# Kernel optimization log

Measured on AMD Instinct MI355X. Metric: run time of the kernel, lower is better.

The kernel has to match this reference:

```python
import jax, jax.numpy as jnp
import numpy as np

NPG = 39      # nodes per graph, from (1+8+64+9)*(39+1)=3280 = lin1 in_features
NEG_SLOPE = 0.2


def gat_conv(x, src, dst, W, a_src, a_dst, b, n):
    """PyG GATConv, heads=1, self-loops already appended to (src, dst).
    x:[N,Fin] W:[Fin,Fout] a_src/a_dst:[Fout] b:[Fout] -> [N,Fout]"""
    h = x @ W                                        # [N,Fout]
    e = jax.nn.leaky_relu(h[src] @ a_src + h[dst] @ a_dst, NEG_SLOPE)  # [E]
    m = jax.lax.stop_gradient(jax.ops.segment_max(e, dst, num_segments=n))
    w = jnp.exp(e - m[dst])
    denom = jax.ops.segment_sum(w, dst, num_segments=n)
    alpha = w / (denom[dst] + 1e-16)                 # segment softmax per target node
    out = jax.ops.segment_sum(alpha[:, None] * h[src], dst, num_segments=n)
    return out + b


def setup_inputs() -> dict:
    key = jax.random.key(0)
    ks = jax.random.split(key, 20)
    B, DEG = 4096, 8
    N = B * NPG
    E = N * DEG
    x = jax.random.normal(ks[0], (N, 1), dtype=jnp.float32)
    # block-diagonal edges: each node emits DEG edges to random nodes in SAME graph
    src = jnp.repeat(jnp.arange(N, dtype=jnp.int64), DEG)
    offs = (src // NPG) * NPG
    dst = offs + jax.random.randint(ks[1], (E,), 0, NPG, dtype=jnp.int64)
    edge_index = jnp.stack([src, dst])
    batch_vec = jnp.repeat(jnp.arange(B, dtype=jnp.int64), NPG)

    def glorot(k, shape):
        fan = shape[0] + (shape[1] if len(shape) > 1 else 1)
        s = jnp.sqrt(6.0 / fan)
        return jax.random.uniform(k, shape, jnp.float32, -s, s)

    p = {
        'W1': glorot(ks[2], (1, 8)),   'a1s': glorot(ks[3], (8,)),  'a1d': glorot(ks[4], (8,)),  'b1': jnp.zeros((8,), jnp.float32),
        'W2': glorot(ks[5], (8, 64)),  'a2s': glorot(ks[6], (64,)), 'a2d': glorot(ks[7], (64,)), 'b2': jnp.zeros((64,), jnp.float32),
        'W3': glorot(ks[8], (64, 9)),  'a3s': glorot(ks[9], (9,)),  'a3d': glorot(ks[10], (9,)), 'b3': jnp.zeros((9,), jnp.float32),
        'lW1': glorot(ks[11], (3280, 5000)), 'lb1': jnp.zeros((5000,), jnp.float32),
        'lW2': glorot(ks[12], (5000, 1024)), 'lb2': jnp.zeros((1024,), jnp.float32),
        'lW3': glorot(ks[13], (1024, 9)),    'lb3': jnp.zeros((9,), jnp.float32),
    }
    return {'x': x, 'edge_index': edge_index, 'batch_vec': batch_vec, **p}


def reference(x, edge_index, batch_vec,
              W1, a1s, a1d, b1, W2, a2s, a2d, b2, W3, a3s, a3d, b3,
              lW1, lb1, lW2, lb2, lW3, lb3):
    N = x.shape[0]
    B = N // NPG
    loops = jnp.arange(N, dtype=edge_index.dtype)
    src = jnp.concatenate([edge_index[0], loops])   # GATConv add_self_loops=True
    dst = jnp.concatenate([edge_index[1], loops])

    res = x.reshape(B, -1)                                    # [B,39]
    out0 = jax.ops.segment_max(x, batch_vec, num_segments=B)  # [B,1]

    h1 = jax.nn.relu(gat_conv(x, src, dst, W1, a1s, a1d, b1, N))   # dropout = eval no-op
    res1 = h1.reshape(B, -1)                                   # [B,312]
    out1 = jax.ops.segment_max(h1, batch_vec, num_segments=B)

    h2 = jax.nn.relu(gat_conv(h1, src, dst, W2, a2s, a2d, b2, N))
    res2 = h2.reshape(B, -1)                                   # [B,2496]
    out2 = jax.ops.segment_max(h2, batch_vec, num_segments=B)

    h3 = jax.nn.relu(gat_conv(h2, src, dst, W3, a3s, a3d, b3, N))
    res3 = h3.reshape(B, -1)                                   # [B,351]
    out3 = jax.ops.segment_max(h3, batch_vec, num_segments=B)

    f = jnp.concatenate([res, res1, res2, res3, out0, out1, out2, out3], axis=1)  # [B,3280]
    f = jax.nn.relu(f @ lW1 + lb1)
    f = jax.nn.relu(f @ lW2 + lb2)
    return f @ lW3 + lb3                                       # [B,9]
```

## Files before the change

### kernel.cpp

```cpp
#include <hip/hip_runtime.h>
#include <hip/hip_bf16.h>
#include <hip/hip_fp16.h>
#include <stdint.h>


typedef float f32x4 __attribute__((ext_vector_type(4)));
typedef short bf16x8 __attribute__((ext_vector_type(8)));

__device__ __forceinline__ unsigned fenc(float f) {
  int s = __float_as_int(f);
  return s < 0 ? ~(unsigned)s : ((unsigned)s | 0x80000000u);
}
__device__ __forceinline__ float fdec(unsigned u) {
  return (u & 0x80000000u) ? __int_as_float((int)(u & 0x7fffffffu))
                           : __int_as_float(~(int)u);
}


__global__ __launch_bounds__(128) void gnn_block(
    const float* __restrict__ x,
    const int* __restrict__ esrc, const int* __restrict__ edst,
    const float* __restrict__ W1, const float* __restrict__ a1s, const float* __restrict__ a1d, const float* __restrict__ b1,
    const float* __restrict__ W2, const float* __restrict__ a2s, const float* __restrict__ a2d, const float* __restrict__ b2,
    const float* __restrict__ W3, const float* __restrict__ a3s, const float* __restrict__ a3d, const float* __restrict__ b3,
    __hip_bfloat16* __restrict__ fA)
{
  __shared__ __align__(16) char HtU[5152];
  __shared__ __align__(16) __half h2buf[2574];
  __shared__ __align__(16) __half h1h[312];
  __shared__ float A[1599];
  __shared__ float den[40];
  __shared__ unsigned umax[40];
  __shared__ float sarr[40], darr[40], xbuf[40];
  __shared__ float a2buf[128];
  __shared__ unsigned umx[132];
  __shared__ float sW3s[576];

  const int tid = threadIdx.x, g = blockIdx.x;
  float* Hf  = (float*)HtU;
  __half* Hh = (__half*)HtU;

  const int rt = g >> 7, mi = (g >> 4) & 7, lrow = g & 15;
  const size_t gbase = (size_t)rt * 52 * 8192 + (size_t)(mi * 2) * 512 + (size_t)lrow * 8;
#define COLADDR(c) (gbase + (size_t)((c) >> 6) * 8192 + (size_t)(((c) >> 5) & 1) * 512 \
                    + (size_t)(((c) >> 3) & 3) * 128 + ((c) & 7))

  for (int i = tid; i < 576; i += 128) sW3s[i] = W3[i];
  a2buf[tid] = (tid < 64) ? a2s[tid] : a2d[tid - 64];
  for (int i = tid; i < 132; i += 128) umx[i] = 0u;
  for (int i = tid; i < 1599; i += 128) A[i] = 0.f;
  if (tid < 39) { den[tid] = 0.f; umax[tid] = 0u; }

  float xv = 0.f;
  if (tid < 39) { xv = x[g * 39 + tid]; xbuf[tid] = xv; fA[COLADDR(tid)] = __float2bfloat16(xv); }

  int els[3], eld[3];
  const int eb = g * 312, nb0 = g * 39;
#pragma unroll
  for (int it = 0; it < 3; ++it) {
    int e = it * 128 + tid, ls = -1, ld = 0;
    if (e < 351) {
      if (e < 312) { ls = esrc[eb + e] - nb0; ld = edst[eb + e] - nb0; }
      else         { ls = e - 312; ld = ls; }
    }
    els[it] = ls; eld[it] = ld;
  }
  float c_s = 0.f, c_d = 0.f;
  float w1r = W1[tid & 7], b1r = b1[tid & 7];
#pragma unroll
  for (int f = 0; f < 8; ++f) { float wv = W1[f]; c_s += wv * a1s[f]; c_d += wv * a1d[f]; }
  __syncthreads();

  if (tid < 39) atomicMax(&umx[0], fenc(xv));
  float ee[3];
#pragma unroll
  for (int it = 0; it < 3; ++it) {
    if (els[it] >= 0) {
      float e = xbuf[els[it]] * c_s + xbuf[eld[it]] * c_d;
      e = (e > 0.f) ? e : 0.2f * e;
      ee[it] = e;
      atomicMax(&umax[eld[it]], fenc(e));
    }
  }
  __syncthreads();
#pragma unroll
  for (int it = 0; it < 3; ++it) {
    if (els[it] >= 0) {
      float wv = __expf(ee[it] - fdec(umax[eld[it]]));
      atomicAdd(&den[eld[it]], wv);
      atomicAdd(&A[eld[it] * 41 + els[it]], wv);
    }
  }
  __syncthreads();
  if (tid < 39) {
    float q = 0.f;
#pragma unroll
    for (int k = 0; k < 39; ++k) q += A[tid * 41 + k] * xbuf[k];
    sarr[tid] = q * (1.f / (den[tid] + 1e-16f));
  }
  __syncthreads();
#pragma unroll
  for (int it = 0; it < 3; ++it) {
    int slot = it * 128 + tid;
    if (slot < 312) {
      int i = slot >> 3, fi = slot & 7;
      float v = fmaxf(sarr[i] * w1r + b1r, 0.f);
      h1h[slot] = __float2half(v);
      fA[COLADDR(39 + slot)] = __float2bfloat16(v);
      atomicMax(&umx[1 + fi], fenc(v));
    }
  }
  __syncthreads();

  {
    const int f = tid & 63, wv2 = tid >> 6;
    float w2k[8];
#pragma unroll
    for (int k = 0; k < 8; ++k) w2k[k] = W2[k * 64 + f];
    for (int it = 0; it < 20; ++it) {
      int i = it * 2 + wv2;
      if (i < 39) {
        float hv = 0.f;
#pragma unroll
        for (int k = 0; k < 8; ++k) hv += __half2float(h1h[i * 8 + k]) * w2k[k];
        Hh[i * 66 + f] = __float2half(hv);
      }
    }
    for (int i = tid; i < 1599; i += 128) A[i] = 0.f;
    if (tid < 39) { den[tid] = 0.f; umax[tid] = 0u; }
    __syncthreads();
    {
      int node = tid & 63;
      if (node < 39) {
        const float* ab = a2buf + (tid & 64);
        float s = 0.f;
#pragma unroll
        for (int f2 = 0; f2 < 64; ++f2) s += __half2float(Hh[node * 66 + f2]) * ab[f2];
        if (tid < 64) sarr[node] = s; else darr[node] = s;
      }
    }
    __syncthreads();
#pragma unroll
    for (int it = 0; it < 3; ++it) {
      if (els[it] >= 0) {
        float e = sarr[els[it]] + darr[eld[it]];
        e = (e > 0.f) ? e : 0.2f * e;
        ee[it] = e;
        atomicMax(&umax[eld[it]], fenc(e));
      }
    }
    __syncthreads();
#pragma unroll
    for (int it = 0; it < 3; ++it) {
      if (els[it] >= 0) {
        float wv = __expf(ee[it] - fdec(umax[eld[it]]));
        atomicAdd(&den[eld[it]], wv);
        atomicAdd(&A[eld[it] * 41 + els[it]], wv);
      }
    }
    __syncthreads();
    const float b2r = b2[f];
    for (int it = 0; it < 20; ++it) {
      int i = it * 2 + wv2;
      if (i < 39) {
        float inv = 1.f / (den[i] + 1e-16f);
        float acc = 0.f;
#pragma unroll
        for (int k = 0; k < 39; ++k) acc += A[i * 41 + k] * __half2float(Hh[k * 66 + f]);
        float v = fmaxf(acc * inv + b2r, 0.f);
        h2buf[i * 66 + f] = __float2half(v);
        fA[COLADDR(351 + i * 64 + f)] = __float2bfloat16(v);
        atomicMax(&umx[9 + f], fenc(v));
      }
    }
  }
  __syncthreads();

  {
#pragma unroll
    for (int it = 0; it < 3; ++it) {
      int slot = it * 128 + tid;
      if (slot < 351) {
        int i = slot / 9, f3 = slot - 9 * i;
        float acc = 0.f;
#pragma unroll
        for (int k = 0; k < 64; ++k) acc += __half2float(h2buf[i * 66 + k]) * sW3s[k * 9 + f3];
        Hf[i * 10 + f3] = acc;
      }
    }
    for (int i = tid; i < 1599; i += 128) A[i] = 0.f;
    if (tid < 39) { den[tid] = 0.f; umax[tid] = 0u; }
    __syncthreads();
    {
      int node = tid & 63;
      if (node < 39) {
        const float* av = (tid < 64) ? a3s : a3d;
        float s = 0.f;
#pragma unroll
        for (int f3 = 0; f3 < 9; ++f3) s += Hf[node * 10 + f3] * av[f3];
        if (tid < 64) sarr[node] = s; else darr[node] = s;
      }
    }
    __syncthreads();
#pragma unroll
    for (int it = 0; it < 3; ++it) {
      if (els[it] >= 0) {
        float e = sarr[els[it]] + darr[eld[it]];
        e = (e > 0.f) ? e : 0.2f * e;
        ee[it] = e;
        atomicMax(&umax[eld[it]], fenc(e));
      }
    }
    __syncthreads();
#pragma unroll
    for (int it = 0; it < 3; ++it) {
      if (els[it] >= 0) {
        float wv = __expf(ee[it] - fdec(umax[eld[it]]));
        atomicAdd(&den[eld[it]], wv);
        atomicAdd(&A[eld[it] * 41 + els[it]], wv);
      }
    }
    __syncthreads();
#pragma unroll
    for (int it = 0; it < 3; ++it) {
      int slot = it * 128 + tid;
      if (slot < 351) {
        int i = slot / 9, f3 = slot - 9 * i;
        float inv = 1.f / (den[i] + 1e-16f);
        float acc = 0.f;
#pragma unroll
        for (int k = 0; k < 39; ++k) acc += A[i * 41 + k] * Hf[k * 10 + f3];
        float v = fmaxf(acc * inv + b3[f3], 0.f);
        fA[COLADDR(2847 + slot)] = __float2bfloat16(v);
        atomicMax(&umx[73 + f3], fenc(v));
      }
    }
  }
  __syncthreads();

  if (tid < 130) {
    int c = 3198 + tid;
    float v = (tid < 82) ? fdec(umx[tid]) : 0.f;
    fA[COLADDR(c)] = __float2bfloat16(v);
  }
#undef COLADDR
}


__global__ __launch_bounds__(256) void conv_tiled(
    const float* __restrict__ W, short* __restrict__ WT,
    int K0, int N0, int KT)
{
  __shared__ float t[64][68];
  const int kb = blockIdx.x * 64, nb = blockIdx.y * 64;
  const int tid = threadIdx.x;
  const int tx = tid & 15, ty = tid >> 4;
#pragma unroll
  for (int r = 0; r < 4; ++r) {
    int k = kb + ty + r * 16, n = nb + tx * 4;
    float4 v = make_float4(0.f, 0.f, 0.f, 0.f);
    if (k < K0 && n < N0) v = *(const float4*)&W[(size_t)k * N0 + n];
    t[ty + r * 16][tx * 4 + 0] = v.x; t[ty + r * 16][tx * 4 + 1] = v.y;
    t[ty + r * 16][tx * 4 + 2] = v.z; t[ty + r * 16][tx * 4 + 3] = v.w;
  }
  __syncthreads();
  const int nl = tid >> 2, kc0 = tid & 3;
#pragma unroll
  for (int h = 0; h < 2; ++h) {
    int kc = kc0 + h * 4;
    int n = nb + nl, k = kb + kc * 8;
    union { bf16x8 v; __hip_bfloat16 b[8]; } z;
#pragma unroll
    for (int j = 0; j < 8; ++j) z.b[j] = __float2bfloat16(t[kc * 8 + j][nl]);
    int rt = n >> 7, mi = (n >> 4) & 7, lr = n & 15;
    int kt = k >> 6, kq = (k >> 5) & 1, lc = (k >> 3) & 3;
    size_t addr = ((((size_t)rt * KT) + kt) * 16 + mi * 2 + kq) * 512 + ((size_t)lr + 16 * lc) * 8;
    *(bf16x8*)&WT[addr] = z.v;
  }
}


__device__ __forceinline__ void gld_lds16(const void* gptr, void* l) {
  typedef const __attribute__((address_space(1))) unsigned int GU;
  typedef __attribute__((address_space(3))) unsigned int LU;
  __builtin_amdgcn_global_load_lds((GU*)gptr, (LU*)l, 16, 0, 0);
}

template<int MODE>
__global__ __launch_bounds__(256) void gemm_tiled(
    const short* __restrict__ A, const short* __restrict__ B,
    const float* __restrict__ bias, int Nreal,
    void* __restrict__ Cout, int Nn, int KT, int ktPerSplit, int outKT)
{
  __shared__ __align__(16) short lA[8192];
  __shared__ __align__(16) short lB[8192];
  const int tid = threadIdx.x;
  const int w = tid >> 6, L = tid & 63;
  const int lrow = L & 15, lch = L >> 4;
  const int mt = blockIdx.y, nt = blockIdx.x;
  const int mw = (w >> 1) * 4, nw = (w & 1) * 4;
  const int kt0 = blockIdx.z * ktPerSplit, kt1 = kt0 + ktPerSplit;

  const short* Ab = A + ((size_t)mt * KT) * 8192 + (size_t)L * 8;
  const short* Bb = B + ((size_t)nt * KT) * 8192 + (size_t)L * 8;

  f32x4 acc[4][4] = {};

  for (int kt = kt0; kt < kt1; ++kt) {
    const short* Ak = Ab + (size_t)kt * 8192;
    const short* Bk = Bb + (size_t)kt * 8192;
#pragma unroll
    for (int j = 0; j < 4; ++j) {
      int st = w * 4 + j;
      gld_lds16(Ak + st * 512, &lA[st * 512]);
      gld_lds16(Bk + st * 512, &lB[st * 512]);
    }
    __syncthreads();
#pragma unroll
    for (int kk = 0; kk < 2; ++kk) {
      bf16x8 af[4], bfr[4];
#pragma unroll
      for (int i = 0; i < 4; ++i) {
        af[i]  = *(const bf16x8*)&lA[((mw + i) * 2 + kk) * 512 + L * 8];
        bfr[i] = *(const bf16x8*)&lB[((nw + i) * 2 + kk) * 512 + L * 8];
      }
#pragma unroll
      for (int i = 0; i < 4; ++i)
#pragma unroll
        for (int j = 0; j < 4; ++j)
          acc[i][j] = __builtin_amdgcn_mfma_f32_16x16x32_bf16(af[i], bfr[j], acc[i][j], 0, 0, 0);
    }
    __syncthreads();
  }

  if (MODE == 0) {
    __hip_bfloat16* C = (__hip_bfloat16*)Cout;
#pragma unroll
    for (int j = 0; j < 4; ++j) {
      int n = nt * 128 + (nw + j) * 16 + lrow;
      float bn = (n < Nreal) ? bias[n] : 0.f;
      int kt = n >> 6, kq = (n >> 5) & 1, lc2 = (n >> 3) & 3, j2 = n & 7;
#pragma unroll
      for (int i = 0; i < 4; ++i) {
        int mi = mw + i;
        size_t base = ((((size_t)mt * outKT + kt) * 16) + mi * 2 + kq) * 512
                      + (size_t)(lch * 4) * 8 + (size_t)lc2 * 128 + j2;
#pragma unroll
        for (int r = 0; r < 4; ++r)
          C[base + r * 8] = __float2bfloat16(fmaxf(acc[i][j][r] + bn, 0.f));
      }
    }
  } else {
    float* P = (float*)Cout + (size_t)blockIdx.z * 4096 * 1024;
#pragma unroll
    for (int j = 0; j < 4; ++j) {
      int n = nt * 128 + (nw + j) * 16 + lrow;
#pragma unroll
      for (int i = 0; i < 4; ++i)
#pragma unroll
        for (int r = 0; r < 4; ++r) {
          int m = mt * 128 + (mw + i) * 16 + lch * 4 + r;
          P[(size_t)m * Nn + n] = acc[i][j][r];
        }
    }
  }
}


__global__ __launch_bounds__(256) void gemm3_fused(
    const float* __restrict__ P,
    const float* __restrict__ b2v,
    const float* __restrict__ W3,
    const float* __restrict__ b3v,
    float* __restrict__ out)
{
  __shared__ float sW3[9 * 1024];
  int tid = threadIdx.x;
  for (int i = tid; i < 9216; i += 256) { int k = i / 9, j = i - 9 * k; sW3[j * 1024 + k] = W3[i]; }
  __syncthreads();
  int row = blockIdx.x * 4 + (tid >> 6);
  int lane = tid & 63;
  const float* p0 = P + (size_t)row * 1024;
  const float* p1 = p0 + (size_t)4096 * 1024;
  float acc[9] = {0, 0, 0, 0, 0, 0, 0, 0, 0};
  for (int t = 0; t < 16; ++t) {
    int k = lane + 64 * t;
    float c = fmaxf(p0[k] + p1[k] + b2v[k], 0.f);
#pragma unroll
    for (int j = 0; j < 9; ++j) acc[j] += c * sW3[j * 1024 + k];
  }
#pragma unroll
  for (int j = 0; j < 9; ++j) {
    float v = acc[j];
    v += __shfl_down(v, 32, 64);
    v += __shfl_down(v, 16, 64);
    v += __shfl_down(v, 8, 64);
    v += __shfl_down(v, 4, 64);
    v += __shfl_down(v, 2, 64);
    v += __shfl_down(v, 1, 64);
    if (lane == 0) out[(size_t)row * 9 + j] = v + b3v[j];
  }
}


extern "C" void kernel_launch(void* const* d_in, const int* in_sizes, int n_in,
                              void* d_out, int out_size, void* d_ws, size_t ws_size,
                              hipStream_t stream)
{
  const float* x   = (const float*)d_in[0];
  const int*   ei  = (const int*)d_in[1];
  const float* W1  = (const float*)d_in[3];
  const float* a1s = (const float*)d_in[4];
  const float* a1d = (const float*)d_in[5];
  const float* b1  = (const float*)d_in[6];
  const float* W2  = (const float*)d_in[7];
  const float* a2s = (const float*)d_in[8];
  const float* a2d = (const float*)d_in[9];
  const float* b2  = (const float*)d_in[10];
  const float* W3  = (const float*)d_in[11];
  const float* a3s = (const float*)d_in[12];
  const float* a3d = (const float*)d_in[13];
  const float* b3  = (const float*)d_in[14];
  const float* lW1 = (const float*)d_in[15];
  const float* lb1 = (const float*)d_in[16];
  const float* lW2 = (const float*)d_in[17];
  const float* lb2 = (const float*)d_in[18];
  const float* lW3 = (const float*)d_in[19];
  const float* lb3 = (const float*)d_in[20];

  const int E = 4096 * 39 * 8;
  const int* esrc = ei;
  const int* edst = ei + E;

  short* fA  = (short*)d_ws;
  short* W1T = fA  + (size_t)4096 * 3328;
  short* C1  = W1T + (size_t)5120 * 3328;
  short* W2T = C1  + (size_t)4096 * 5120;
  float* P   = (float*)d_ws;

  conv_tiled<<<dim3(3328 / 64, 5120 / 64), 256, 0, stream>>>(lW1, W1T, 3280, 5000, 52);
  conv_tiled<<<dim3(5120 / 64, 1024 / 64), 256, 0, stream>>>(lW2, W2T, 5000, 1024, 80);
  gnn_block<<<4096, 128, 0, stream>>>(x, esrc, edst,
                                      W1, a1s, a1d, b1, W2, a2s, a2d, b2, W3, a3s, a3d, b3,
                                      (__hip_bfloat16*)fA);
  gemm_tiled<0><<<dim3(40, 32, 1), 256, 0, stream>>>(fA, W1T, lb1, 5000, C1, 5120, 52, 52, 80);
  gemm_tiled<1><<<dim3(8, 32, 2), 256, 0, stream>>>(C1, W2T, nullptr, 1024, P, 1024, 80, 40, 0);
  gemm3_fused<<<1024, 256, 0, stream>>>(P, lb2, lW3, lb3, (float*)d_out);
}
```

Baseline: 502.7 us.

## Vectorize GAT block LDS accesses with padded, transposed layouts and register-held features

Reorganizes the per-graph GNN kernel's shared memory. Attention rows are padded to 44 floats and zeroed with 16-byte stores, layer-3 features and W3 are stored transposed, and the inner dot products read f32x4/f16x8 vectors instead of scalars. Layer-2 projected features are kept in a 40-entry register array per thread, so aggregation reads them from registers rather than LDS. The aim is fewer LDS instructions in the small-matrix loops of the GAT stage, at the cost of more registers and slightly more shared memory, which could lower occupancy.

New measurement: 492.3 us. 2.1% less time.

```diff
diff --git a/kernel.cpp b/kernel.cpp
--- a/kernel.cpp
+++ b/kernel.cpp
@@ -6,6 +6,7 @@
 
 typedef float f32x4 __attribute__((ext_vector_type(4)));
 typedef short bf16x8 __attribute__((ext_vector_type(8)));
+typedef _Float16 f16x8 __attribute__((ext_vector_type(8)));
 
 __device__ __forceinline__ unsigned fenc(float f) {
   int s = __float_as_int(f);
@@ -25,31 +26,32 @@
     const float* __restrict__ W3, const float* __restrict__ a3s, const float* __restrict__ a3d, const float* __restrict__ b3,
     __hip_bfloat16* __restrict__ fA)
 {
-  __shared__ __align__(16) char HtU[5152];
-  __shared__ __align__(16) __half h2buf[2574];
-  __shared__ __align__(16) __half h1h[312];
-  __shared__ float A[1599];
-  __shared__ float den[40];
+  __shared__ __align__(16) float A[1720];
+  __shared__ __align__(16) __half Hh2[2816];
+  __shared__ __align__(16) __half h1h[320];
+  __shared__ __align__(16) float HfT[400];
+  __shared__ __align__(16) float sW3T[616];
+  __shared__ __align__(16) float xbuf[40];
+  __shared__ __align__(16) float a2buf[128];
+  __shared__ float sarr[40], darr[40], den[40];
   __shared__ unsigned umax[40];
-  __shared__ float sarr[40], darr[40], xbuf[40];
-  __shared__ float a2buf[128];
   __shared__ unsigned umx[132];
-  __shared__ float sW3s[576];
-
-  const int tid = threadIdx.x, g = blockIdx.x;
-  float* Hf  = (float*)HtU;
-  __half* Hh = (__half*)HtU;
+  __shared__ float a3sb[12], a3db[12], b3b[12];
+
+  const int tid = threadIdx.x, g = blockIdx.x, w = tid >> 6, f = tid & 63;
 
   const int rt = g >> 7, mi = (g >> 4) & 7, lrow = g & 15;
   const size_t gbase = (size_t)rt * 52 * 8192 + (size_t)(mi * 2) * 512 + (size_t)lrow * 8;
 #define COLADDR(c) (gbase + (size_t)((c) >> 6) * 8192 + (size_t)(((c) >> 5) & 1) * 512 \
                     + (size_t)(((c) >> 3) & 3) * 128 + ((c) & 7))
 
-  for (int i = tid; i < 576; i += 128) sW3s[i] = W3[i];
+  for (int i = tid; i < 576; i += 128) { int k = i / 9, f3 = i - 9 * k; sW3T[f3 * 68 + k] = W3[i]; }
   a2buf[tid] = (tid < 64) ? a2s[tid] : a2d[tid - 64];
+  if (tid < 9) { a3sb[tid] = a3s[tid]; a3db[tid] = a3d[tid]; b3b[tid] = b3[tid]; }
   for (int i = tid; i < 132; i += 128) umx[i] = 0u;
-  for (int i = tid; i < 1599; i += 128) A[i] = 0.f;
-  if (tid < 39) { den[tid] = 0.f; umax[tid] = 0u; }
+  for (int i = tid; i < 430; i += 128) *(f32x4*)&A[i * 4] = (f32x4){0.f, 0.f, 0.f, 0.f};
+  for (int i = tid; i < 400; i += 128) HfT[i] = 0.f;
+  if (tid < 40) { den[tid] = 0.f; umax[tid] = 0u; xbuf[tid] = 0.f; }
 
   float xv = 0.f;
   if (tid < 39) { xv = x[g * 39 + tid]; xbuf[tid] = xv; fA[COLADDR(tid)] = __float2bfloat16(xv); }
@@ -66,9 +68,9 @@
     els[it] = ls; eld[it] = ld;
   }
   float c_s = 0.f, c_d = 0.f;
-  float w1r = W1[tid & 7], b1r = b1[tid & 7];
-#pragma unroll
-  for (int f = 0; f < 8; ++f) { float wv = W1[f]; c_s += wv * a1s[f]; c_d += wv * a1d[f]; }
+  const float w1r = W1[tid & 7], b1r = b1[tid & 7];
+#pragma unroll
+  for (int ff = 0; ff < 8; ++ff) { float wv = W1[ff]; c_s += wv * a1s[ff]; c_d += wv * a1d[ff]; }
   __syncthreads();
 
   if (tid < 39) atomicMax(&umx[0], fenc(xv));
@@ -88,14 +90,19 @@
     if (els[it] >= 0) {
       float wv = __expf(ee[it] - fdec(umax[eld[it]]));
       atomicAdd(&den[eld[it]], wv);
-      atomicAdd(&A[eld[it] * 41 + els[it]], wv);
+      atomicAdd(&A[eld[it] * 44 + els[it]], wv);
     }
   }
   __syncthreads();
   if (tid < 39) {
+    const float* Ar = &A[tid * 44];
     float q = 0.f;
 #pragma unroll
-    for (int k = 0; k < 39; ++k) q += A[tid * 41 + k] * xbuf[k];
+    for (int c = 0; c < 10; ++c) {
+      f32x4 a4 = *(const f32x4*)&Ar[c * 4];
+      f32x4 x4 = *(const f32x4*)&xbuf[c * 4];
+      q += a4.x * x4.x + a4.y * x4.y + a4.z * x4.z + a4.w * x4.w;
+    }
     sarr[tid] = q * (1.f / (den[tid] + 1e-16f));
   }
   __syncthreads();
@@ -112,63 +119,82 @@
   }
   __syncthreads();
 
+  float ht2r[40];
   {
-    const int f = tid & 63, wv2 = tid >> 6;
     float w2k[8];
 #pragma unroll
     for (int k = 0; k < 8; ++k) w2k[k] = W2[k * 64 + f];
-    for (int it = 0; it < 20; ++it) {
-      int i = it * 2 + wv2;
-      if (i < 39) {
-        float hv = 0.f;
-#pragma unroll
-        for (int k = 0; k < 8; ++k) hv += __half2float(h1h[i * 8 + k]) * w2k[k];
-        Hh[i * 66 + f] = __float2half(hv);
-      }
-    }
-    for (int i = tid; i < 1599; i += 128) A[i] = 0.f;
+#pragma unroll
+    for (int i = 0; i < 39; ++i) {
+      f16x8 hr = *(const f16x8*)&h1h[i * 8];
+      float hv = 0.f;
+#pragma unroll
+      for (int k = 0; k < 8; ++k) hv += (float)hr[k] * w2k[k];
+      ht2r[i] = hv;
+    }
+    ht2r[39] = 0.f;
+#pragma unroll
+    for (int i = 0; i < 39; ++i) {
+      if ((i < 20) ? (w == 0) : (w == 1))
+        Hh2[i * 72 + f] = __float2half(ht2r[i]);
+    }
+    for (int i = tid; i < 430; i += 128) *(f32x4*)&A[i * 4] = (f32x4){0.f, 0.f, 0.f, 0.f};
     if (tid < 39) { den[tid] = 0.f; umax[tid] = 0u; }
-    __syncthreads();
-    {
-      int node = tid & 63;
-      if (node < 39) {
-        const float* ab = a2buf + (tid & 64);
-        float s = 0.f;
-#pragma unroll
-        for (int f2 = 0; f2 < 64; ++f2) s += __half2float(Hh[node * 66 + f2]) * ab[f2];
-        if (tid < 64) sarr[node] = s; else darr[node] = s;
-      }
-    }
-    __syncthreads();
-#pragma unroll
-    for (int it = 0; it < 3; ++it) {
-      if (els[it] >= 0) {
-        float e = sarr[els[it]] + darr[eld[it]];
-        e = (e > 0.f) ? e : 0.2f * e;
-        ee[it] = e;
-        atomicMax(&umax[eld[it]], fenc(e));
-      }
-    }
-    __syncthreads();
-#pragma unroll
-    for (int it = 0; it < 3; ++it) {
-      if (els[it] >= 0) {
-        float wv = __expf(ee[it] - fdec(umax[eld[it]]));
-        atomicAdd(&den[eld[it]], wv);
-        atomicAdd(&A[eld[it] * 41 + els[it]], wv);
-      }
-    }
-    __syncthreads();
+  }
+  __syncthreads();
+  {
+    int node = f;
+    if (node < 39) {
+      const float* ab = a2buf + (tid & 64);
+      const __half* hr = &Hh2[node * 72];
+      float s = 0.f;
+#pragma unroll
+      for (int c = 0; c < 8; ++c) {
+        f16x8 hv = *(const f16x8*)&hr[c * 8];
+        f32x4 a0 = *(const f32x4*)&ab[c * 8];
+        f32x4 a1 = *(const f32x4*)&ab[c * 8 + 4];
+        s += (float)hv[0] * a0.x + (float)hv[1] * a0.y + (float)hv[2] * a0.z + (float)hv[3] * a0.w
+           + (float)hv[4] * a1.x + (float)hv[5] * a1.y + (float)hv[6] * a1.z + (float)hv[7] * a1.w;
+      }
+      if (tid < 64) sarr[node] = s; else darr[node] = s;
+    }
+  }
+  __syncthreads();
+#pragma unroll
+  for (int it = 0; it < 3; ++it) {
+    if (els[it] >= 0) {
+      float e = sarr[els[it]] + darr[eld[it]];
+      e = (e > 0.f) ? e : 0.2f * e;
+      ee[it] = e;
+      atomicMax(&umax[eld[it]], fenc(e));
+    }
+  }
+  __syncthreads();
+#pragma unroll
+  for (int it = 0; it < 3; ++it) {
+    if (els[it] >= 0) {
+      float wv = __expf(ee[it] - fdec(umax[eld[it]]));
+      atomicAdd(&den[eld[it]], wv);
+      atomicAdd(&A[eld[it] * 44 + els[it]], wv);
+    }
+  }
+  __syncthreads();
+  {
     const float b2r = b2[f];
     for (int it = 0; it < 20; ++it) {
-      int i = it * 2 + wv2;
+      int i = it * 2 + w;
       if (i < 39) {
         float inv = 1.f / (den[i] + 1e-16f);
+        const float* Ar = &A[i * 44];
         float acc = 0.f;
 #pragma unroll
-        for (int k = 0; k < 39; ++k) acc += A[i * 41 + k] * __half2float(Hh[k * 66 + f]);
+        for (int c = 0; c < 10; ++c) {
+          f32x4 a4 = *(const f32x4*)&Ar[c * 4];
+          acc += a4.x * ht2r[c * 4] + a4.y * ht2r[c * 4 + 1]
+               + a4.z * ht2r[c * 4 + 2] + a4.w * ht2r[c * 4 + 3];
+        }
         float v = fmaxf(acc * inv + b2r, 0.f);
-        h2buf[i * 66 + f] = __float2half(v);
+        Hh2[i * 72 + f] = __float2half(v);
         fA[COLADDR(351 + i * 64 + f)] = __float2bfloat16(v);
         atomicMax(&umx[9 + f], fenc(v));
       }
@@ -182,58 +208,72 @@
       int slot = it * 128 + tid;
       if (slot < 351) {
         int i = slot / 9, f3 = slot - 9 * i;
+        const __half* hr = &Hh2[i * 72];
+        const float* wr = &sW3T[f3 * 68];
         float acc = 0.f;
 #pragma unroll
-        for (int k = 0; k < 64; ++k) acc += __half2float(h2buf[i * 66 + k]) * sW3s[k * 9 + f3];
-        Hf[i * 10 + f3] = acc;
-      }
-    }
-    for (int i = tid; i < 1599; i += 128) A[i] = 0.f;
+        for (int c = 0; c < 8; ++c) {
+          f16x8 hv = *(const f16x8*)&hr[c * 8];
+          f32x4 w0 = *(const f32x4*)&wr[c * 8];
+          f32x4 w1 = *(const f32x4*)&wr[c * 8 + 4];
+          acc += (float)hv[0] * w0.x + (float)hv[1] * w0.y + (float)hv[2] * w0.z + (float)hv[3] * w0.w
+               + (float)hv[4] * w1.x + (float)hv[5] * w1.y + (float)hv[6] * w1.z + (float)hv[7] * w1.w;
+        }
+        HfT[f3 * 44 + i] = acc;
+      }
+    }
+    for (int i = tid; i < 430; i += 128) *(f32x4*)&A[i * 4] = (f32x4){0.f, 0.f, 0.f, 0.f};
     if (tid < 39) { den[tid] = 0.f; umax[tid] = 0u; }
-    __syncthreads();
-    {
-      int node = tid & 63;
-      if (node < 39) {
-        const float* av = (tid < 64) ? a3s : a3d;
-        float s = 0.f;
-#pragma unroll
-        for (int f3 = 0; f3 < 9; ++f3) s += Hf[node * 10 + f3] * av[f3];
-        if (tid < 64) sarr[node] = s; else darr[node] = s;
-      }
-    }
-    __syncthreads();
-#pragma unroll
-    for (int it = 0; it < 3; ++it) {
-      if (els[it] >= 0) {
-        float e = sarr[els[it]] + darr[eld[it]];
-        e = (e > 0.f) ? e : 0.2f * e;
-        ee[it] = e;
-        atomicMax(&umax[eld[it]], fenc(e));
-      }
-    }
-    __syncthreads();
-#pragma unroll
-    for (int it = 0; it < 3; ++it) {
-      if (els[it] >= 0) {
-        float wv = __expf(ee[it] - fdec(umax[eld[it]]));
-        atomicAdd(&den[eld[it]], wv);
-        atomicAdd(&A[eld[it] * 41 + els[it]], wv);
-      }
-    }
-    __syncthreads();
-#pragma unroll
-    for (int it = 0; it < 3; ++it) {
-      int slot = it * 128 + tid;
-      if (slot < 351) {
-        int i = slot / 9, f3 = slot - 9 * i;
-        float inv = 1.f / (den[i] + 1e-16f);
-        float acc = 0.f;
-#pragma unroll
-        for (int k = 0; k < 39; ++k) acc += A[i * 41 + k] * Hf[k * 10 + f3];
-        float v = fmaxf(acc * inv + b3[f3], 0.f);
-        fA[COLADDR(2847 + slot)] = __float2bfloat16(v);
-        atomicMax(&umx[73 + f3], fenc(v));
-      }
+  }
+  __syncthreads();
+  {
+    int node = f;
+    if (node < 39) {
+      const float* av = (tid < 64) ? a3sb : a3db;
+      float s = 0.f;
+#pragma unroll
+      for (int f3 = 0; f3 < 9; ++f3) s += HfT[f3 * 44 + node] * av[f3];
+      if (tid < 64) sarr[node] = s; else darr[node] = s;
+    }
+  }
+  __syncthreads();
+#pragma unroll
+  for (int it = 0; it < 3; ++it) {
+    if (els[it] >= 0) {
+      float e = sarr[els[it]] + darr[eld[it]];
+      e = (e > 0.f) ? e : 0.2f * e;
+      ee[it] = e;
+      atomicMax(&umax[eld[it]], fenc(e));
+    }
+  }
+  __syncthreads();
+#pragma unroll
+  for (int it = 0; it < 3; ++it) {
+    if (els[it] >= 0) {
+      float wv = __expf(ee[it] - fdec(umax[eld[it]]));
+      atomicAdd(&den[eld[it]], wv);
+      atomicAdd(&A[eld[it] * 44 + els[it]], wv);
+    }
+  }
+  __syncthreads();
+#pragma unroll
+  for (int it = 0; it < 3; ++it) {
+    int slot = it * 128 + tid;
+    if (slot < 351) {
+      int i = slot / 9, f3 = slot - 9 * i;
+      float inv = 1.f / (den[i] + 1e-16f);
+      const float* Ar = &A[i * 44];
+      const float* Hr = &HfT[f3 * 44];
+      float acc = 0.f;
+#pragma unroll
+      for (int c = 0; c < 10; ++c) {
+        f32x4 a4 = *(const f32x4*)&Ar[c * 4];
+        f32x4 h4 = *(const f32x4*)&Hr[c * 4];
+        acc += a4.x * h4.x + a4.y * h4.y + a4.z * h4.z + a4.w * h4.w;
+      }
+      float v = fmaxf(acc * inv + b3b[f3], 0.f);
+      fA[COLADDR(2847 + slot)] = __float2bfloat16(v);
+      atomicMax(&umx[73 + f3], fenc(v));
     }
   }
   __syncthreads();
```
